# Kernel tuning notes

Hardware: AMD Instinct MI355X
Metric: run time of the kernel (lower is better)

## Reference

```python
import math
import jax, jax.numpy as jnp
import numpy as np

B, T, C = 4, 2048, 1024

def setup_inputs() -> dict:
    key = jax.random.key(0)
    k1, k2 = jax.random.split(key)
    x = jax.random.normal(k1, (B, T, C), dtype=jnp.float32)
    W_kqv = jax.random.normal(k2, (C, 3 * C), dtype=jnp.float32) * 0.02
    return {"x": x, "W_kqv": W_kqv}

def reference(x, W_kqv):
    Bq, Tq, Cq = x.shape
    qkv = jnp.einsum('btc,cd->btd', x, W_kqv)            # [B,T,3C]
    q, k, v = jnp.split(qkv, 3, axis=2)                   # each [B,T,C]
    # scaled scores: note scale is 1/sqrt(n_embed), matching the source
    attn = jnp.einsum('btc,bsc->bts', q, k) / math.sqrt(Cq)  # [B,T,T]
    mask = jnp.tril(jnp.ones((Tq, Tq), dtype=bool))
    attn = jnp.where(mask, attn, -jnp.inf)
    attn = jax.nn.softmax(attn, axis=-1)
    y = jnp.einsum('bts,bsc->btc', attn, v)               # [B,T,C]
    return y
```

## Files before the change

kernel.cpp:

```cpp
#include <hip/hip_runtime.h>

typedef unsigned short u16;
typedef __bf16 bf16x8 __attribute__((ext_vector_type(8)));
typedef float f32x4 __attribute__((ext_vector_type(4)));

#define Bb 4
#define Tt 2048
#define Cc 1024

#define GLOAD_LDS16(g, l)                                                     \
  __builtin_amdgcn_global_load_lds(                                           \
      (const __attribute__((address_space(1))) void*)(g),                     \
      (__attribute__((address_space(3))) void*)(l), 16, 0, 0)

__device__ inline u16 f2bf(float f) {
  unsigned u = __builtin_bit_cast(unsigned, f);
  unsigned r = u + 0x7fffu + ((u >> 16) & 1u);
  return (u16)(r >> 16);
}

__global__ __launch_bounds__(256) void cast_f32_bf16_vec4(
    const float* __restrict__ in, u16* __restrict__ out, int n4) {
  int i = blockIdx.x * 256 + threadIdx.x;
  if (i >= n4) return;
  float4 v = reinterpret_cast<const float4*>(in)[i];
  ushort4 o;
  o.x = f2bf(v.x); o.y = f2bf(v.y); o.z = f2bf(v.z); o.w = f2bf(v.w);
  reinterpret_cast<ushort4*>(out)[i] = o;
}

__global__ __launch_bounds__(256) void transpose_cast_w(
    const float* __restrict__ W, u16* __restrict__ Wt) {
  __shared__ float tile[32][33];
  int n0 = blockIdx.x * 32;
  int k0 = blockIdx.y * 32;
  int tx = threadIdx.x;
  int ty = threadIdx.y;
#pragma unroll
  for (int i = 0; i < 4; i++)
    tile[ty + i * 8][tx] = W[(size_t)(k0 + ty + i * 8) * 3072 + n0 + tx];
  __syncthreads();
#pragma unroll
  for (int i = 0; i < 4; i++)
    Wt[(size_t)(n0 + ty + i * 8) * 1024 + k0 + tx] = f2bf(tile[tx][ty + i * 8]);
}

template <int MODE>
__global__ __launch_bounds__(256) void gemm_bt(
    const u16* __restrict__ A0, const u16* __restrict__ B0,
    size_t sAbatch, size_t sBbatch,
    int K, int lda, int ldb,
    u16* __restrict__ qO, u16* __restrict__ kO, u16* __restrict__ vTO,
    float* __restrict__ SO, float* __restrict__ YO) {
  int bx = blockIdx.x, by = blockIdx.y, bz = blockIdx.z;
  if (MODE == 1 && bx > by) return;

  const u16* A = A0 + (size_t)bz * sAbatch + (size_t)by * 128 * lda;
  const u16* Bt = B0 + (size_t)bz * sBbatch + (size_t)bx * 128 * ldb;
  int kEnd = (MODE == 2) ? min(K, (by + 1) * 128) : K;

  __shared__ __attribute__((aligned(16))) u16 As[128 * 32];
  __shared__ __attribute__((aligned(16))) u16 Bs[128 * 32];

  int tid = threadIdx.x;
  int lane = tid & 63, w = tid >> 6;
  int wr = (w >> 1) * 64, wc = (w & 1) * 64;
  int row16 = lane & 15, kq = (lane >> 4) * 8;

  int r0 = w * 16 + (lane >> 2);
  int c0 = (lane & 3) * 8;

  f32x4 acc[4][4] = {};

  for (int kt = 0; kt < kEnd; kt += 32) {
    const u16* Ag = A + (size_t)r0 * lda + kt + c0;
    const u16* Bg = Bt + (size_t)r0 * ldb + kt + c0;
    GLOAD_LDS16(Ag, &As[w * 512]);
    GLOAD_LDS16(Ag + (size_t)64 * lda, &As[2048 + w * 512]);
    GLOAD_LDS16(Bg, &Bs[w * 512]);
    GLOAD_LDS16(Bg + (size_t)64 * ldb, &Bs[2048 + w * 512]);
    __syncthreads();

    bf16x8 a[4], b[4];
#pragma unroll
    for (int m = 0; m < 4; m++)
      a[m] = *reinterpret_cast<const bf16x8*>(&As[(wr + m * 16 + row16) * 32 + kq]);
#pragma unroll
    for (int n = 0; n < 4; n++)
      b[n] = *reinterpret_cast<const bf16x8*>(&Bs[(wc + n * 16 + row16) * 32 + kq]);
#pragma unroll
    for (int m = 0; m < 4; m++)
#pragma unroll
      for (int n = 0; n < 4; n++)
        acc[m][n] = __builtin_amdgcn_mfma_f32_16x16x32_bf16(a[m], b[n], acc[m][n], 0, 0, 0);
    __syncthreads();
  }

  int colf = lane & 15, rbase = (lane >> 4) * 4;
#pragma unroll
  for (int i = 0; i < 4; i++) {
#pragma unroll
    for (int j = 0; j < 4; j++) {
#pragma unroll
      for (int r = 0; r < 4; r++) {
        int m = by * 128 + wr + i * 16 + rbase + r;
        int n = bx * 128 + wc + j * 16 + colf;
        float v = acc[i][j][r];
        if (MODE == 0) {
          int seg = n >> 10, cn = n & 1023;
          int b = m >> 11, t = m & 2047;
          u16 hv = f2bf(v);
          if (seg == 0)
            qO[(((size_t)(b * Tt + t)) << 10) + cn] = hv;
          else if (seg == 1)
            kO[(((size_t)(b * Tt + t)) << 10) + cn] = hv;
          else
            vTO[((size_t)(b * Cc + cn)) * Tt + t] = hv;
        } else if (MODE == 1) {
          SO[((size_t)bz * Tt + m) * Tt + n] = v * 0.03125f;
        } else {
          YO[((size_t)bz * Tt + m) * Cc + n] = v;
        }
      }
    }
  }
}

__global__ __launch_bounds__(256) void softmax_rows(
    const float* __restrict__ S, u16* __restrict__ P) {
  int rowi = blockIdx.x;
  int i = rowi & (Tt - 1);
  const float* s = S + (size_t)rowi * Tt;
  u16* p = P + (size_t)rowi * Tt;
  int len = i + 1;
  int tid = threadIdx.x;
  __shared__ float red[256];

  float m = -1e30f;
  for (int j = tid; j < len; j += 256) m = fmaxf(m, s[j]);
  red[tid] = m;
  __syncthreads();
  for (int st = 128; st > 0; st >>= 1) {
    if (tid < st) red[tid] = fmaxf(red[tid], red[tid + st]);
    __syncthreads();
  }
  m = red[0];
  __syncthreads();

  float l = 0.f;
  for (int j = tid; j < len; j += 256) l += __expf(s[j] - m);
  red[tid] = l;
  __syncthreads();
  for (int st = 128; st > 0; st >>= 1) {
    if (tid < st) red[tid] += red[tid + st];
    __syncthreads();
  }
  l = red[0];
  float inv = 1.0f / l;

  for (int j = tid; j < len; j += 256) p[j] = f2bf(__expf(s[j] - m) * inv);
  for (int j = len + tid; j < Tt; j += 256) p[j] = 0;
}

extern "C" void kernel_launch(void* const* d_in, const int* in_sizes, int n_in,
                              void* d_out, int out_size, void* d_ws, size_t ws_size,
                              hipStream_t stream) {
  const float* x = (const float*)d_in[0];
  const float* W = (const float*)d_in[1];
  float* Y = (float*)d_out;

  char* ws = (char*)d_ws;
  size_t off = 0;
  auto carve = [&](size_t bytes) -> void* {
    void* p = ws + off;
    off += (bytes + 255) & ~(size_t)255;
    return p;
  };
  u16* xb = (u16*)carve((size_t)Bb * Tt * Cc * 2);
  u16* wt = (u16*)carve((size_t)3 * Cc * Cc * 2);
  u16* qb = (u16*)carve((size_t)Bb * Tt * Cc * 2);
  u16* kb = (u16*)carve((size_t)Bb * Tt * Cc * 2);
  u16* vT = (u16*)carve((size_t)Bb * Cc * Tt * 2);
  float* S = (float*)carve((size_t)Bb * Tt * Tt * 4);
  u16* P = (u16*)carve((size_t)Bb * Tt * Tt * 2);

  cast_f32_bf16_vec4<<<(Bb * Tt * Cc / 4 + 255) / 256, 256, 0, stream>>>(
      x, xb, Bb * Tt * Cc / 4);
  transpose_cast_w<<<dim3(96, 32), dim3(32, 8), 0, stream>>>(W, wt);
  gemm_bt<0><<<dim3(24, 64, 1), 256, 0, stream>>>(
      xb, wt, 0, 0, Cc, Cc, Cc, qb, kb, vT, nullptr, nullptr);
  gemm_bt<1><<<dim3(16, 16, 4), 256, 0, stream>>>(
      qb, kb, (size_t)Tt * Cc, (size_t)Tt * Cc, Cc, Cc, Cc,
      nullptr, nullptr, nullptr, S, nullptr);
  softmax_rows<<<Bb * Tt, 256, 0, stream>>>(S, P);
  gemm_bt<2><<<dim3(8, 16, 4), 256, 0, stream>>>(
      P, vT, (size_t)Tt * Tt, (size_t)Cc * Tt, Tt, Tt, Tt,
      nullptr, nullptr, nullptr, nullptr, Y);
}
```

Before: 330.6 us.

## Replace QKV projection GEMM with 256x256 tiled, pipelined, swizzled-LDS kernel

Adds a dedicated QKV projection kernel using 256x256 output tiles with 512 threads. It prefetches K-slices into swizzled LDS buffers through direct global-to-LDS loads, overlaps those loads with MFMA work using manual vmcnt waits, barriers and setprio, and swaps the generic MODE 0 path for it. The goal is more data reuse per tile and hidden global-load latency in the largest dense GEMM. In exchange it brings heavy manual synchronisation and large LDS and register use, and the grid shrinks to 384 blocks.

```diff
diff --git a/kernel.cpp b/kernel.cpp
--- a/kernel.cpp
+++ b/kernel.cpp
@@ -12,6 +12,9 @@
   __builtin_amdgcn_global_load_lds(                                           \
       (const __attribute__((address_space(1))) void*)(g),                     \
       (__attribute__((address_space(3))) void*)(l), 16, 0, 0)
+
+#define WAITV8 asm volatile("s_waitcnt vmcnt(8)" ::: "memory")
+#define WAITV0 asm volatile("s_waitcnt vmcnt(0)" ::: "memory")
 
 __device__ inline u16 f2bf(float f) {
   unsigned u = __builtin_bit_cast(unsigned, f);
@@ -45,12 +48,153 @@
     Wt[(size_t)(n0 + ty + i * 8) * 1024 + k0 + tx] = f2bf(tile[tx][ty + i * 8]);
 }
 
+
+__device__ __forceinline__ void stage_unit(const u16* __restrict__ G, int ld,
+                                           u16* lds_unit, int tid) {
+#pragma unroll
+  for (int j = 0; j < 2; j++) {
+    int u = j * 8192 + tid * 16;
+    int l = u ^ (((u >> 7) & 7) << 4);
+    int grow = l >> 6;
+    int gcol = (l & 63) >> 1;
+    GLOAD_LDS16(G + (size_t)grow * ld + gcol, lds_unit + (u >> 1));
+  }
+}
+
+__device__ __forceinline__ bf16x8 lds_frag(const u16* unit, int row, int fq) {
+  int off = row * 64 + fq * 16;
+  off ^= ((off >> 7) & 7) << 4;
+  return *reinterpret_cast<const bf16x8*>(
+      reinterpret_cast<const char*>(unit) + off);
+}
+
+__global__ __launch_bounds__(512, 2) void gemm256_qkv(
+    const u16* __restrict__ A0, const u16* __restrict__ B0,
+    u16* __restrict__ qO, u16* __restrict__ kO, u16* __restrict__ vTO) {
+  const int K = Cc, lda = Cc, ldb = Cc, NT = K / 64;
+  int bx = blockIdx.x, by = blockIdx.y;
+
+  const u16* A = A0 + (size_t)by * 256 * lda;
+  const u16* Bt = B0 + (size_t)bx * 256 * ldb;
+
+  __shared__ __attribute__((aligned(16))) u16 lds[4][2][8192];
+
+  int tid = threadIdx.x;
+  int lane = tid & 63, w = tid >> 6;
+  int wm = (w >> 2) * 128, wn = (w & 3) * 64;
+  int fr = lane & 15, fq = lane >> 4;
+
+  f32x4 acc[8][4] = {};
+
+  stage_unit(A + 0, lda, &lds[0][0][0], tid);
+  stage_unit(Bt + 0, ldb, &lds[2][0][0], tid);
+  stage_unit(A + 32, lda, &lds[1][0][0], tid);
+  stage_unit(Bt + 32, ldb, &lds[3][0][0], tid);
+  stage_unit(A + 64, lda, &lds[0][1][0], tid);
+  stage_unit(Bt + 64, ldb, &lds[2][1][0], tid);
+  WAITV8;
+  __builtin_amdgcn_s_barrier();
+
+  for (int t = 0; t < NT; ++t) {
+    int par = t & 1;
+    int parn = par ^ 1;
+    bool st1 = (t + 1 < NT);
+    bool st2 = (t + 2 < NT);
+    bool tail = (t >= NT - 2);
+    bf16x8 a[4], b[4];
+
+#pragma unroll
+    for (int mi = 0; mi < 4; mi++)
+      a[mi] = lds_frag(&lds[0][par][0], wm + mi * 16 + fr, fq);
+#pragma unroll
+    for (int ni = 0; ni < 4; ni++)
+      b[ni] = lds_frag(&lds[2][par][0], wn + ni * 16 + fr, fq);
+    if (st1) stage_unit(A + (t + 1) * 64 + 32, lda, &lds[1][parn][0], tid);
+    __builtin_amdgcn_s_barrier();
+    __builtin_amdgcn_s_setprio(1);
+#pragma unroll
+    for (int mi = 0; mi < 4; mi++)
+#pragma unroll
+      for (int ni = 0; ni < 4; ni++)
+        acc[mi][ni] = __builtin_amdgcn_mfma_f32_16x16x32_bf16(a[mi], b[ni], acc[mi][ni], 0, 0, 0);
+    __builtin_amdgcn_s_setprio(0);
+    __builtin_amdgcn_s_barrier();
+
+#pragma unroll
+    for (int mi = 0; mi < 4; mi++)
+      a[mi] = lds_frag(&lds[0][par][0], wm + 64 + mi * 16 + fr, fq);
+    if (st1) stage_unit(Bt + (t + 1) * 64 + 32, ldb, &lds[3][parn][0], tid);
+    __builtin_amdgcn_s_barrier();
+    __builtin_amdgcn_s_setprio(1);
+#pragma unroll
+    for (int mi = 0; mi < 4; mi++)
+#pragma unroll
+      for (int ni = 0; ni < 4; ni++)
+        acc[4 + mi][ni] = __builtin_amdgcn_mfma_f32_16x16x32_bf16(a[mi], b[ni], acc[4 + mi][ni], 0, 0, 0);
+    __builtin_amdgcn_s_setprio(0);
+    if (tail) { WAITV0; } else { WAITV8; }
+    __builtin_amdgcn_s_barrier();
+
+#pragma unroll
+    for (int mi = 0; mi < 4; mi++)
+      a[mi] = lds_frag(&lds[1][par][0], wm + mi * 16 + fr, fq);
+#pragma unroll
+    for (int ni = 0; ni < 4; ni++)
+      b[ni] = lds_frag(&lds[3][par][0], wn + ni * 16 + fr, fq);
+    if (st2) stage_unit(A + (t + 2) * 64, lda, &lds[0][par][0], tid);
+    __builtin_amdgcn_s_barrier();
+    __builtin_amdgcn_s_setprio(1);
+#pragma unroll
+    for (int mi = 0; mi < 4; mi++)
+#pragma unroll
+      for (int ni = 0; ni < 4; ni++)
+        acc[mi][ni] = __builtin_amdgcn_mfma_f32_16x16x32_bf16(a[mi], b[ni], acc[mi][ni], 0, 0, 0);
+    __builtin_amdgcn_s_setprio(0);
+    __builtin_amdgcn_s_barrier();
+
+#pragma unroll
+    for (int mi = 0; mi < 4; mi++)
+      a[mi] = lds_frag(&lds[1][par][0], wm + 64 + mi * 16 + fr, fq);
+    if (st2) stage_unit(Bt + (t + 2) * 64, ldb, &lds[2][par][0], tid);
+    __builtin_amdgcn_s_barrier();
+    __builtin_amdgcn_s_setprio(1);
+#pragma unroll
+    for (int mi = 0; mi < 4; mi++)
+#pragma unroll
+      for (int ni = 0; ni < 4; ni++)
+        acc[4 + mi][ni] = __builtin_amdgcn_mfma_f32_16x16x32_bf16(a[mi], b[ni], acc[4 + mi][ni], 0, 0, 0);
+    __builtin_amdgcn_s_setprio(0);
+    if (tail) { WAITV0; } else { WAITV8; }
+    __builtin_amdgcn_s_barrier();
+  }
+
+#pragma unroll
+  for (int mi = 0; mi < 8; mi++) {
+#pragma unroll
+    for (int ni = 0; ni < 4; ni++) {
+#pragma unroll
+      for (int r = 0; r < 4; r++) {
+        int m = by * 256 + wm + mi * 16 + fq * 4 + r;
+        int n = bx * 256 + wn + ni * 16 + fr;
+        u16 hv = f2bf(acc[mi][ni][r]);
+        int seg = n >> 10, cn = n & 1023;
+        int b = m >> 11, tt = m & 2047;
+        if (seg == 0)
+          qO[(((size_t)(b * Tt + tt)) << 10) + cn] = hv;
+        else if (seg == 1)
+          kO[(((size_t)(b * Tt + tt)) << 10) + cn] = hv;
+        else
+          vTO[((size_t)(b * Cc + cn)) * Tt + tt] = hv;
+      }
+    }
+  }
+}
+
 template <int MODE>
 __global__ __launch_bounds__(256) void gemm_bt(
     const u16* __restrict__ A0, const u16* __restrict__ B0,
     size_t sAbatch, size_t sBbatch,
     int K, int lda, int ldb,
-    u16* __restrict__ qO, u16* __restrict__ kO, u16* __restrict__ vTO,
     float* __restrict__ SO, float* __restrict__ YO) {
   int bx = blockIdx.x, by = blockIdx.y, bz = blockIdx.z;
   if (MODE == 1 && bx > by) return;
@@ -106,17 +250,7 @@
         int m = by * 128 + wr + i * 16 + rbase + r;
         int n = bx * 128 + wc + j * 16 + colf;
         float v = acc[i][j][r];
-        if (MODE == 0) {
-          int seg = n >> 10, cn = n & 1023;
-          int b = m >> 11, t = m & 2047;
-          u16 hv = f2bf(v);
-          if (seg == 0)
-            qO[(((size_t)(b * Tt + t)) << 10) + cn] = hv;
-          else if (seg == 1)
-            kO[(((size_t)(b * Tt + t)) << 10) + cn] = hv;
-          else
-            vTO[((size_t)(b * Cc + cn)) * Tt + t] = hv;
-        } else if (MODE == 1) {
+        if (MODE == 1) {
           SO[((size_t)bz * Tt + m) * Tt + n] = v * 0.03125f;
         } else {
           YO[((size_t)bz * Tt + m) * Cc + n] = v;
@@ -187,13 +321,10 @@
   cast_f32_bf16_vec4<<<(Bb * Tt * Cc / 4 + 255) / 256, 256, 0, stream>>>(
       x, xb, Bb * Tt * Cc / 4);
   transpose_cast_w<<<dim3(96, 32), dim3(32, 8), 0, stream>>>(W, wt);
-  gemm_bt<0><<<dim3(24, 64, 1), 256, 0, stream>>>(
-      xb, wt, 0, 0, Cc, Cc, Cc, qb, kb, vT, nullptr, nullptr);
+  gemm256_qkv<<<dim3(12, 32), 512, 0, stream>>>(xb, wt, qb, kb, vT);
   gemm_bt<1><<<dim3(16, 16, 4), 256, 0, stream>>>(
-      qb, kb, (size_t)Tt * Cc, (size_t)Tt * Cc, Cc, Cc, Cc,
-      nullptr, nullptr, nullptr, S, nullptr);
+      qb, kb, (size_t)Tt * Cc, (size_t)Tt * Cc, Cc, Cc, Cc, S, nullptr);
   softmax_rows<<<Bb * Tt, 256, 0, stream>>>(S, P);
   gemm_bt<2><<<dim3(8, 16, 4), 256, 0, stream>>>(
-      P, vT, (size_t)Tt * Tt, (size_t)Cc * Tt, Tt, Tt, Tt,
-      nullptr, nullptr, nullptr, nullptr, Y);
-}
+      P, vT, (size_t)Tt * Tt, (size_t)Cc * Tt, Tt, Tt, Tt, nullptr, Y);
+}
```

Result: faster. 322.3 us (-2.5%).
